# Performance work log

Hardware: AMD Instinct MI355X
Metric: run time of the kernel (lower is better)

The kernel has to match this reference:

```python
import jax, jax.numpy as jnp
import numpy as np

N_NODES = 1_000_000
N_GRAPHS = 8192
DIM = 64
FEAT = 64


def setup_inputs() -> dict:
    key = jax.random.key(0)
    ks = jax.random.split(key, 12)
    s = 0.05
    inp = {}
    inp["x"] = jax.random.normal(ks[0], (N_NODES, FEAT), jnp.float32)
    inp["batch"] = jnp.sort(jax.random.randint(ks[1], (N_NODES,), 0, N_GRAPHS, dtype=jnp.int32))
    inp["lin0_w"] = jax.random.normal(ks[2], (DIM, FEAT), jnp.float32) * s
    inp["lin0_b"] = jnp.zeros((DIM,), jnp.float32)
    inp["lin1_w"] = jax.random.normal(ks[3], (DIM, DIM), jnp.float32) * s
    inp["lin1_b"] = jnp.zeros((DIM,), jnp.float32)
    inp["gru_wih"] = jax.random.normal(ks[4], (3 * DIM, DIM), jnp.float32) * s
    inp["gru_whh"] = jax.random.normal(ks[5], (3 * DIM, DIM), jnp.float32) * s
    inp["gru_bih"] = jnp.zeros((3 * DIM,), jnp.float32)
    inp["gru_bhh"] = jnp.zeros((3 * DIM,), jnp.float32)
    inp["lstm_wih"] = jax.random.normal(ks[6], (4 * DIM, 2 * DIM), jnp.float32) * s
    inp["lstm_whh"] = jax.random.normal(ks[7], (4 * DIM, DIM), jnp.float32) * s
    inp["lstm_bih"] = jnp.zeros((4 * DIM,), jnp.float32)
    inp["lstm_bhh"] = jnp.zeros((4 * DIM,), jnp.float32)
    inp["lin2_w"] = jax.random.normal(ks[8], (DIM, 2 * DIM), jnp.float32) * s
    inp["lin2_b"] = jnp.zeros((DIM,), jnp.float32)
    inp["lin3_w"] = jax.random.normal(ks[9], (1, DIM), jnp.float32) * s
    inp["lin3_b"] = jnp.zeros((1,), jnp.float32)
    inp["n_graphs"] = N_GRAPHS
    return inp


def _gru_step(m, h, wih, whh, bih, bhh):
    # single-step PyTorch GRU semantics
    gi = m @ wih.T + bih          # [N, 3D]
    gh = h @ whh.T + bhh          # [N, 3D]
    ir, iz, in_ = jnp.split(gi, 3, axis=-1)
    hr, hz, hn = jnp.split(gh, 3, axis=-1)
    r = jax.nn.sigmoid(ir + hr)
    z = jax.nn.sigmoid(iz + hz)
    n = jnp.tanh(in_ + r * hn)
    return (1.0 - z) * n + z * h


def _segment_softmax(e, batch, n_graphs):
    m = jax.ops.segment_max(e, batch, num_segments=n_graphs)
    ex = jnp.exp(e - m[batch])
    s = jax.ops.segment_sum(ex, batch, num_segments=n_graphs)
    return ex / (s[batch] + 1e-16)


def reference(x, batch, lin0_w, lin0_b, lin1_w, lin1_b,
              gru_wih, gru_whh, gru_bih, gru_bhh,
              lstm_wih, lstm_whh, lstm_bih, lstm_bhh,
              lin2_w, lin2_b, lin3_w, lin3_b, n_graphs):
    dim = lin0_w.shape[0]
    out = jax.nn.relu(x @ lin0_w.T + lin0_b)   # [N, D]
    h = out
    for _ in range(3):
        m = jax.nn.relu(out @ lin1_w.T + lin1_b)
        h = _gru_step(m, h, gru_wih, gru_whh, gru_bih, gru_bhh)
        out = h

    # Set2Set, processing_steps = 3
    q_star = jnp.zeros((n_graphs, 2 * dim), out.dtype)
    hl = jnp.zeros((n_graphs, dim), out.dtype)
    cl = jnp.zeros((n_graphs, dim), out.dtype)
    for _ in range(3):
        gates = q_star @ lstm_wih.T + lstm_bih + hl @ lstm_whh.T + lstm_bhh  # [B, 4D]
        gi, gf, gg, go = jnp.split(gates, 4, axis=-1)
        cl = jax.nn.sigmoid(gf) * cl + jax.nn.sigmoid(gi) * jnp.tanh(gg)
        hl = jax.nn.sigmoid(go) * jnp.tanh(cl)
        q = hl                                   # [B, D]
        e = jnp.sum(out * q[batch], axis=-1)     # [N]
        a = _segment_softmax(e, batch, n_graphs) # [N]
        r = jax.ops.segment_sum(a[:, None] * out, batch, num_segments=n_graphs)  # [B, D]
        q_star = jnp.concatenate([q, r], axis=-1)

    y = jax.nn.relu(q_star @ lin2_w.T + lin2_b)
    y = y @ lin3_w.T + lin3_b
    return y.reshape(-1)
```

## Files before the change

kernel.cpp:

```cpp
#include <hip/hip_runtime.h>
#include <hip/hip_bf16.h>
#include <math.h>

#define TILES 8
#define MBLK 128

typedef __attribute__((ext_vector_type(8))) short bf8;
typedef __attribute__((ext_vector_type(4))) float f32x4;

#define MFMA(a, b, c) __builtin_amdgcn_mfma_f32_16x16x32_bf16(a, b, c, 0, 0, 0)

__device__ __forceinline__ float fast_rcp(float x) { return __builtin_amdgcn_rcpf(x); }
#if __has_builtin(__builtin_amdgcn_exp2f)
__device__ __forceinline__ float exp2b(float x) { return __builtin_amdgcn_exp2f(x); }
#else
__device__ __forceinline__ float exp2b(float x) { return exp2f(x); }
#endif
__device__ __forceinline__ float sigm2(float xp) { return fast_rcp(1.0f + exp2b(-xp)); }
__device__ __forceinline__ float tanh2s(float up) {
    return fmaf(2.0f, fast_rcp(1.0f + exp2b(-up)), -1.0f);
}
__device__ __forceinline__ float sigm(float x) { return fast_rcp(1.0f + __expf(-x)); }
__device__ __forceinline__ float tanh2(float x) { return fmaf(2.0f, fast_rcp(1.0f + __expf(-2.0f * x)), -1.0f); }

__device__ __forceinline__ unsigned short f2bf(float v) {
    union { __hip_bfloat16 b; unsigned short u; } cv;
    cv.b = __float2bfloat16(v);
    return cv.u;
}
__device__ __forceinline__ float bf2f(unsigned short u) {
    union { unsigned short u; __hip_bfloat16 b; } cv;
    cv.u = u;
    return __bfloat162float(cv.b);
}
__device__ __forceinline__ void split_tr(float v, unsigned short& hi, unsigned short& lo) {
    unsigned int uv = __builtin_bit_cast(unsigned int, v);
    hi = (unsigned short)(uv >> 16);
    float rem = v - __builtin_bit_cast(float, uv & 0xffff0000u);
    lo = f2bf(rem);
}
__device__ __forceinline__ f32x4 ntload4(const float* p) {
    return __builtin_nontemporal_load((const f32x4*)p);
}

__global__ void prep_kernel(const float* __restrict__ l0w, const float* __restrict__ l1w,
                            const float* __restrict__ gwih, const float* __restrict__ gwhh,
                            const float* __restrict__ lwih, const float* __restrict__ lwhh,
                            const float* __restrict__ l2w,
                            const int* __restrict__ batch,
                            unsigned short* __restrict__ whi, unsigned short* __restrict__ wlo,
                            float* __restrict__ liT, float* __restrict__ lhT,
                            float* __restrict__ l2T,
                            int* __restrict__ startp,
                            int n_nodes, int n_graphs)
{
    int tid = blockIdx.x * 256 + threadIdx.x;
    if (tid < 32768) {
        int e = tid & 7, lane = (tid >> 3) & 63, ks = (tid >> 9) & 1, jt = tid >> 10;
        const float* W; int jl;
        if (jt < 4)       { W = l0w;  jl = jt; }
        else if (jt < 8)  { W = l1w;  jl = jt - 4; }
        else if (jt < 20) { W = gwih; jl = jt - 8; }
        else              { W = gwhh; jl = jt - 20; }
        int j = jl * 16 + (lane & 15);
        int k = ks * 32 + (lane >> 4) * 8 + e;
        float v = W[j * 64 + k];
        if (jt >= 8) v *= (j < 128) ? 1.44269504f : 2.88539008f;
        unsigned short hi = f2bf(v);
        whi[tid] = hi;
        wlo[tid] = f2bf(v - bf2f(hi));
    }
    if (tid < 32768) liT[tid] = lwih[(tid & 255) * 128 + (tid >> 8)];
    if (tid < 16384) lhT[tid] = lwhh[(tid & 255) * 64 + (tid >> 8)];
    if (tid < 8192)  l2T[tid] = l2w[(tid & 63) * 128 + (tid >> 6)];
    if (tid <= n_graphs) {
        int lo = 0, hi = n_nodes;
        while (lo < hi) {
            int mid = (lo + hi) >> 1;
            if (batch[mid] < tid) lo = mid + 1; else hi = mid;
        }
        startp[tid] = lo;
    }
}

__launch_bounds__(256, 2)
__global__ void node_kernel(const float* __restrict__ x,
                            const unsigned short* __restrict__ whi,
                            const unsigned short* __restrict__ wlo,
                            const float* __restrict__ l0b, const float* __restrict__ l1b,
                            const float* __restrict__ gbih, const float* __restrict__ gbhh,
                            float* __restrict__ outv, int n_nodes)
{
    __shared__ unsigned short MHI[TILES * 1024], MLO[TILES * 1024];
    __shared__ unsigned short HHI[TILES * 1024], HLO[TILES * 1024];
    const int tid = threadIdx.x;
    const int w = tid >> 6, lane = tid & 63, c = lane & 15, g = lane >> 4;
    const long node0 = (long)blockIdx.x * MBLK;
    const int j = w * 16 + c;

    const float bR  = (gbih[j] + gbhh[j]) * 1.44269504f;
    const float bZ  = (gbih[64 + j] + gbhh[64 + j]) * 1.44269504f;
    const float bNI = gbih[128 + j] * 2.88539008f;
    const float bNH = gbhh[128 + j] * 2.88539008f;
    const float bL1 = l1b[j];
    const float bL0 = l0b[j];

    const int kgj = (j >> 3) & 3;
    const int koff2 = ((j >> 5) * 512) + (kgj * 128) + (j & 7);
    const int lane_swz = (lane & 48) | (c ^ g);

    const bf8* WH = (const bf8*)whi;
    const bf8* WL = (const bf8*)wlo;
#define LF(name, jt) \
    bf8 name##h0 = WH[((jt) * 2 + 0) * 64 + lane], name##h1 = WH[((jt) * 2 + 1) * 64 + lane], \
        name##l0 = WL[((jt) * 2 + 0) * 64 + lane], name##l1 = WL[((jt) * 2 + 1) * 64 + lane];
    LF(w0, w)
    LF(w1, 4 + w)
    LF(gir, 8 + w)  LF(giz, 12 + w)  LF(gin, 16 + w)
    LF(ghr, 20 + w) LF(ghz, 24 + w) LF(ghn, 28 + w)
#undef LF

    float hc[TILES][4];

#pragma unroll
    for (int t = 0; t < TILES; ++t) {
        long nd = node0 + t * 16 + c;
        if (nd >= n_nodes) nd = n_nodes - 1;
        const float* xp = x + nd * 64 + g * 8;
        float va[8], vb[8];
        {
            float4 u0 = *(const float4*)xp;
            float4 u1 = *(const float4*)(xp + 4);
            float4 u2 = *(const float4*)(xp + 32);
            float4 u3 = *(const float4*)(xp + 36);
            va[0] = u0.x; va[1] = u0.y; va[2] = u0.z; va[3] = u0.w;
            va[4] = u1.x; va[5] = u1.y; va[6] = u1.z; va[7] = u1.w;
            vb[0] = u2.x; vb[1] = u2.y; vb[2] = u2.z; vb[3] = u2.w;
            vb[4] = u3.x; vb[5] = u3.y; vb[6] = u3.z; vb[7] = u3.w;
        }
        bf8 xh0, xl0, xh1, xl1;
#pragma unroll
        for (int e = 0; e < 8; ++e) {
            unsigned short h0, l0, h1, l1;
            split_tr(va[e], h0, l0);
            split_tr(vb[e], h1, l1);
            xh0[e] = (short)h0; xl0[e] = (short)l0;
            xh1[e] = (short)h1; xl1[e] = (short)l1;
        }
        f32x4 acc = {bL0, bL0, bL0, bL0};
        acc = MFMA(xh0, w0h0, acc); acc = MFMA(xl0, w0h0, acc); acc = MFMA(xh0, w0l0, acc);
        acc = MFMA(xh1, w0h1, acc); acc = MFMA(xl1, w0h1, acc); acc = MFMA(xh1, w0l1, acc);
#pragma unroll
        for (int p = 0; p < 4; ++p) {
            float hv = fmaxf(acc[p], 0.0f);
            hc[t][p] = hv;
            int r = g * 4 + p;
            unsigned short hi, lo;
            split_tr(hv, hi, lo);
            int idx = t * 1024 + koff2 + ((r ^ kgj) << 3);
            HHI[idx] = hi;
            HLO[idx] = lo;
        }
    }
    __syncthreads();

    for (int iter = 0; iter < 3; ++iter) {
#pragma unroll
        for (int t = 0; t < TILES; ++t) {
            const bf8* hh = (const bf8*)&HHI[t * 1024];
            const bf8* hl = (const bf8*)&HLO[t * 1024];
            bf8 ah0 = hh[lane_swz], ah1 = hh[64 + lane_swz];
            bf8 al0 = hl[lane_swz], al1 = hl[64 + lane_swz];
            f32x4 acc = {bL1, bL1, bL1, bL1};
            acc = MFMA(ah0, w1h0, acc); acc = MFMA(al0, w1h0, acc); acc = MFMA(ah0, w1l0, acc);
            acc = MFMA(ah1, w1h1, acc); acc = MFMA(al1, w1h1, acc); acc = MFMA(ah1, w1l1, acc);
#pragma unroll
            for (int p = 0; p < 4; ++p) {
                float mv = fmaxf(acc[p], 0.0f);
                int r = g * 4 + p;
                unsigned short hi, lo;
                split_tr(mv, hi, lo);
                int idx = t * 1024 + koff2 + ((r ^ kgj) << 3);
                MHI[idx] = hi;
                MLO[idx] = lo;
            }
        }
        __syncthreads();

#pragma unroll
        for (int t = 0; t < TILES; ++t) {
            const bf8* mh = (const bf8*)&MHI[t * 1024];
            const bf8* ml = (const bf8*)&MLO[t * 1024];
            const bf8* hh = (const bf8*)&HHI[t * 1024];
            const bf8* hl = (const bf8*)&HLO[t * 1024];
            bf8 amh0 = mh[lane_swz], amh1 = mh[64 + lane_swz];
            bf8 aml0 = ml[lane_swz], aml1 = ml[64 + lane_swz];
            bf8 ahh0 = hh[lane_swz], ahh1 = hh[64 + lane_swz];
            bf8 ahl0 = hl[lane_swz], ahl1 = hl[64 + lane_swz];

            f32x4 aR  = {bR, bR, bR, bR};
            f32x4 aZ  = {bZ, bZ, bZ, bZ};
            f32x4 aNI = {bNI, bNI, bNI, bNI};
            f32x4 aNH = {bNH, bNH, bNH, bNH};

            aR = MFMA(amh0, girh0, aR); aR = MFMA(aml0, girh0, aR); aR = MFMA(amh0, girl0, aR);
            aR = MFMA(amh1, girh1, aR); aR = MFMA(aml1, girh1, aR); aR = MFMA(amh1, girl1, aR);
            aR = MFMA(ahh0, ghrh0, aR); aR = MFMA(ahl0, ghrh0, aR); aR = MFMA(ahh0, ghrl0, aR);
            aR = MFMA(ahh1, ghrh1, aR); aR = MFMA(ahl1, ghrh1, aR); aR = MFMA(ahh1, ghrl1, aR);

            aZ = MFMA(amh0, gizh0, aZ); aZ = MFMA(aml0, gizh0, aZ); aZ = MFMA(amh0, gizl0, aZ);
            aZ = MFMA(amh1, gizh1, aZ); aZ = MFMA(aml1, gizh1, aZ); aZ = MFMA(amh1, gizl1, aZ);
            aZ = MFMA(ahh0, ghzh0, aZ); aZ = MFMA(ahl0, ghzh0, aZ); aZ = MFMA(ahh0, ghzl0, aZ);
            aZ = MFMA(ahh1, ghzh1, aZ); aZ = MFMA(ahl1, ghzh1, aZ); aZ = MFMA(ahh1, ghzl1, aZ);

            aNI = MFMA(amh0, ginh0, aNI); aNI = MFMA(aml0, ginh0, aNI); aNI = MFMA(amh0, ginl0, aNI);
            aNI = MFMA(amh1, ginh1, aNI); aNI = MFMA(aml1, ginh1, aNI); aNI = MFMA(amh1, ginl1, aNI);

            aNH = MFMA(ahh0, ghnh0, aNH); aNH = MFMA(ahl0, ghnh0, aNH); aNH = MFMA(ahh0, ghnl0, aNH);
            aNH = MFMA(ahh1, ghnh1, aNH); aNH = MFMA(ahl1, ghnh1, aNH); aNH = MFMA(ahh1, ghnl1, aNH);

#pragma unroll
            for (int p = 0; p < 4; ++p) {
                float rg = sigm2(aR[p]);
                float zg = sigm2(aZ[p]);
                float ng = tanh2s(fmaf(rg, aNH[p], aNI[p]));
                hc[t][p] = fmaf(zg, hc[t][p] - ng, ng);
            }
        }

        if (iter < 2) {
            __syncthreads();
#pragma unroll
            for (int t = 0; t < TILES; ++t)
#pragma unroll
                for (int p = 0; p < 4; ++p) {
                    int r = g * 4 + p;
                    unsigned short hi, lo;
                    split_tr(hc[t][p], hi, lo);
                    int idx = t * 1024 + koff2 + ((r ^ kgj) << 3);
                    HHI[idx] = hi;
                    HLO[idx] = lo;
                }
            __syncthreads();
        }
    }

#pragma unroll
    for (int t = 0; t < TILES; ++t)
#pragma unroll
        for (int p = 0; p < 4; ++p) {
            long nd = node0 + t * 16 + g * 4 + p;
            if (nd < n_nodes) outv[nd * 64 + j] = hc[t][p];
        }
}

__global__ void s2s_kernel(const float* __restrict__ outv,
                           const int* __restrict__ startp,
                           const float* __restrict__ liT, const float* __restrict__ lhT,
                           const float* __restrict__ lbih, const float* __restrict__ lbhh,
                           const float* __restrict__ l2T, const float* __restrict__ l2b,
                           const float* __restrict__ l3w, const float* __restrict__ l3b,
                           float* __restrict__ yout, int n_graphs)
{
    __shared__ float uS[4][192];
    __shared__ float clS[4][64];
    __shared__ float mG[16], sG[16];
    __shared__ float rG[16][64];

    const int t = threadIdx.x;
    const int w = t >> 6, lane = t & 63;
    const int gbase = blockIdx.x * 4;
    const int grp = t >> 4, l = t & 15;

    uS[w][lane] = 0.0f; uS[w][64 + lane] = 0.0f; uS[w][128 + lane] = 0.0f;
    clS[w][lane] = 0.0f;
    __syncthreads();

    for (int step = 0; step < 3; ++step) {
        {
            const int d = lane;
            float aI = lbih[d]       + lbhh[d];
            float aF = lbih[64 + d]  + lbhh[64 + d];
            float aG = lbih[128 + d] + lbhh[128 + d];
            float aO = lbih[192 + d] + lbhh[192 + d];
            for (int k = 0; k < 128; ++k) {
                float uv = uS[w][k];
                const float* wr = liT + k * 256;
                aI = fmaf(wr[d], uv, aI);
                aF = fmaf(wr[64 + d], uv, aF);
                aG = fmaf(wr[128 + d], uv, aG);
                aO = fmaf(wr[192 + d], uv, aO);
            }
            for (int k = 0; k < 64; ++k) {
                float hv = uS[w][128 + k];
                const float* wr = lhT + k * 256;
                aI = fmaf(wr[d], hv, aI);
                aF = fmaf(wr[64 + d], hv, aF);
                aG = fmaf(wr[128 + d], hv, aG);
                aO = fmaf(wr[192 + d], hv, aO);
            }
            float c = sigm(aF) * clS[w][d] + sigm(aI) * tanh2(aG);
            clS[w][d] = c;
            float h = sigm(aO) * tanh2(c);
            uS[w][d] = h;
            uS[w][128 + d] = h;
        }
        __syncthreads();

        for (int idx = 0; idx < 4; ++idx) {
            const int g = gbase + idx;
            int s0 = 0, cnt = 0;
            if (g < n_graphs) { s0 = startp[g]; cnt = startp[g + 1] - s0; }

            const float q0 = uS[idx][l * 4 + 0], q1 = uS[idx][l * 4 + 1];
            const float q2 = uS[idx][l * 4 + 2], q3 = uS[idx][l * 4 + 3];

            float m = -INFINITY, s = 0.0f;
            float r0 = 0.0f, r1 = 0.0f, r2 = 0.0f, r3 = 0.0f;

            int n = grp;
            for (; n + 16 < cnt; n += 32) {
                f32x4 va = ntload4(outv + (size_t)(s0 + n) * 64 + l * 4);
                f32x4 vb = ntload4(outv + (size_t)(s0 + n + 16) * 64 + l * 4);
                float ea = fmaf(va.x, q0, fmaf(va.y, q1, fmaf(va.z, q2, va.w * q3)));
                float eb = fmaf(vb.x, q0, fmaf(vb.y, q1, fmaf(vb.z, q2, vb.w * q3)));
#pragma unroll
                for (int o = 1; o < 16; o <<= 1) {
                    ea += __shfl_xor(ea, o);
                    eb += __shfl_xor(eb, o);
                }
                float mn = fmaxf(m, fmaxf(ea, eb));
                float sc = __expf(m - mn);
                float wa = __expf(ea - mn);
                float wb = __expf(eb - mn);
                s = s * sc + wa + wb;
                r0 = fmaf(r0, sc, fmaf(wa, va.x, wb * vb.x));
                r1 = fmaf(r1, sc, fmaf(wa, va.y, wb * vb.y));
                r2 = fmaf(r2, sc, fmaf(wa, va.z, wb * vb.z));
                r3 = fmaf(r3, sc, fmaf(wa, va.w, wb * vb.w));
                m = mn;
            }
            if (n < cnt) {
                f32x4 va = ntload4(outv + (size_t)(s0 + n) * 64 + l * 4);
                float ea = fmaf(va.x, q0, fmaf(va.y, q1, fmaf(va.z, q2, va.w * q3)));
#pragma unroll
                for (int o = 1; o < 16; o <<= 1) ea += __shfl_xor(ea, o);
                float mn = fmaxf(m, ea);
                float sc = __expf(m - mn);
                float wa = __expf(ea - mn);
                s = s * sc + wa;
                r0 = fmaf(r0, sc, wa * va.x);
                r1 = fmaf(r1, sc, wa * va.y);
                r2 = fmaf(r2, sc, wa * va.z);
                r3 = fmaf(r3, sc, wa * va.w);
                m = mn;
            }

            if (l == 0) { mG[grp] = m; sG[grp] = s; }
            rG[grp][l * 4 + 0] = r0;
            rG[grp][l * 4 + 1] = r1;
            rG[grp][l * 4 + 2] = r2;
            rG[grp][l * 4 + 3] = r3;
            __syncthreads();

            if (t < 64) {
                float M = -INFINITY;
#pragma unroll
                for (int j2 = 0; j2 < 16; ++j2) M = fmaxf(M, mG[j2]);
                float out;
                if (M == -INFINITY) {
                    out = 0.0f;
                } else {
                    float ssum = 0.0f, racc = 0.0f;
#pragma unroll
                    for (int j2 = 0; j2 < 16; ++j2) {
                        float sc = __expf(mG[j2] - M);
                        ssum = fmaf(sG[j2], sc, ssum);
                        racc = fmaf(rG[j2][t], sc, racc);
                    }
                    out = racc / (ssum + 1e-16f);
                }
                uS[idx][64 + t] = out;
            }
            __syncthreads();
        }
    }

    {
        const int d = lane;
        float a0 = l2b[d], a1 = 0.0f, a2 = 0.0f, a3 = 0.0f;
        for (int k = 0; k < 128; k += 4) {
            a0 = fmaf(l2T[(k + 0) * 64 + d], uS[w][k + 0], a0);
            a1 = fmaf(l2T[(k + 1) * 64 + d], uS[w][k + 1], a1);
            a2 = fmaf(l2T[(k + 2) * 64 + d], uS[w][k + 2], a2);
            a3 = fmaf(l2T[(k + 3) * 64 + d], uS[w][k + 3], a3);
        }
        float y = fmaxf((a0 + a1) + (a2 + a3), 0.0f);
        float p = l3w[d] * y;
#pragma unroll
        for (int o = 32; o > 0; o >>= 1) p += __shfl_xor(p, o);
        if (d == 0 && gbase + w < n_graphs) yout[gbase + w] = p + l3b[0];
    }
}

extern "C" void kernel_launch(void* const* d_in, const int* in_sizes, int n_in,
                              void* d_out, int out_size, void* d_ws, size_t ws_size,
                              hipStream_t stream)
{
    const float* x     = (const float*)d_in[0];
    const int*   batch = (const int*)d_in[1];
    const float* l0w   = (const float*)d_in[2];
    const float* l0b   = (const float*)d_in[3];
    const float* l1w   = (const float*)d_in[4];
    const float* l1b   = (const float*)d_in[5];
    const float* gwih  = (const float*)d_in[6];
    const float* gwhh  = (const float*)d_in[7];
    const float* gbih  = (const float*)d_in[8];
    const float* gbhh  = (const float*)d_in[9];
    const float* lwih  = (const float*)d_in[10];
    const float* lwhh  = (const float*)d_in[11];
    const float* lbih  = (const float*)d_in[12];
    const float* lbhh  = (const float*)d_in[13];
    const float* l2w   = (const float*)d_in[14];
    const float* l2b   = (const float*)d_in[15];
    const float* l3w   = (const float*)d_in[16];
    const float* l3b   = (const float*)d_in[17];

    const int n_nodes  = in_sizes[1];
    const int n_graphs = out_size;

    float* wsf = (float*)d_ws;
    float* outv = wsf;
    float* liT  = wsf + (size_t)n_nodes * 64;
    float* lhT  = liT + 32768;
    float* l2T  = lhT + 16384;
    unsigned short* whi = (unsigned short*)(l2T + 8192);
    unsigned short* wlo = whi + 32768;
    int* startp = (int*)(wlo + 32768);

    prep_kernel<<<128, 256, 0, stream>>>(l0w, l1w, gwih, gwhh, lwih, lwhh, l2w, batch,
                                         whi, wlo, liT, lhT, l2T, startp,
                                         n_nodes, n_graphs);
    node_kernel<<<(n_nodes + MBLK - 1) / MBLK, 256, 0, stream>>>(
        x, whi, wlo, l0b, l1b, gbih, gbhh, outv, n_nodes);
    s2s_kernel<<<(n_graphs + 3) / 4, 256, 0, stream>>>(
        outv, startp, liT, lhT, lbih, lbhh, l2T, l2b, l3w, l3b,
        (float*)d_out, n_graphs);
}
```

Baseline: 768.5 us.

## Transpose MFMA operands so each lane owns four contiguous features for vector stores

Swaps the A/B operands of every MFMA so the accumulator holds four consecutive output features per lane instead of four nodes. This lets the hi/lo bf16 split results be written to shared memory as one short4 store instead of four scalar stores. It also lets the final output be written as one float4 global store per tile rather than scattered scalar stores. The shared-memory layout changes to an unswizzled one, which risks bank conflicts on the packed writes and on the bf8 reads.

```diff
diff --git a/kernel.cpp b/kernel.cpp
--- a/kernel.cpp
+++ b/kernel.cpp
@@ -96,18 +96,22 @@
     const int tid = threadIdx.x;
     const int w = tid >> 6, lane = tid & 63, c = lane & 15, g = lane >> 4;
     const long node0 = (long)blockIdx.x * MBLK;
-    const int j = w * 16 + c;
-
-    const float bR  = (gbih[j] + gbhh[j]) * 1.44269504f;
-    const float bZ  = (gbih[64 + j] + gbhh[64 + j]) * 1.44269504f;
-    const float bNI = gbih[128 + j] * 2.88539008f;
-    const float bNH = gbhh[128 + j] * 2.88539008f;
-    const float bL1 = l1b[j];
-    const float bL0 = l0b[j];
-
-    const int kgj = (j >> 3) & 3;
-    const int koff2 = ((j >> 5) * 512) + (kgj * 128) + (j & 7);
-    const int lane_swz = (lane & 48) | (c ^ g);
+    const int j0 = w * 16 + g * 4;
+
+    const float LOG2E = 1.44269504f;
+    float bR[4], bZ[4], bNI[4], bNH[4], bL0[4], bL1[4];
+#pragma unroll
+    for (int p = 0; p < 4; ++p) {
+        bR[p]  = (gbih[j0 + p] + gbhh[j0 + p]) * LOG2E;
+        bZ[p]  = (gbih[64 + j0 + p] + gbhh[64 + j0 + p]) * LOG2E;
+        bNI[p] = gbih[128 + j0 + p] * (2.0f * LOG2E);
+        bNH[p] = gbhh[128 + j0 + p] * (2.0f * LOG2E);
+        bL0[p] = l0b[j0 + p];
+        bL1[p] = l1b[j0 + p];
+    }
+
+    const int waddr = ((w >> 1) * 512) + (((w & 1) * 2 + (g >> 1)) * 128)
+                    + (c * 8) + ((g & 1) * 4);
 
     const bf8* WH = (const bf8*)whi;
     const bf8* WL = (const bf8*)wlo;
@@ -147,20 +151,18 @@
             xh0[e] = (short)h0; xl0[e] = (short)l0;
             xh1[e] = (short)h1; xl1[e] = (short)l1;
         }
-        f32x4 acc = {bL0, bL0, bL0, bL0};
-        acc = MFMA(xh0, w0h0, acc); acc = MFMA(xl0, w0h0, acc); acc = MFMA(xh0, w0l0, acc);
-        acc = MFMA(xh1, w0h1, acc); acc = MFMA(xl1, w0h1, acc); acc = MFMA(xh1, w0l1, acc);
+        f32x4 acc = {bL0[0], bL0[1], bL0[2], bL0[3]};
+        acc = MFMA(w0h0, xh0, acc); acc = MFMA(w0h0, xl0, acc); acc = MFMA(w0l0, xh0, acc);
+        acc = MFMA(w0h1, xh1, acc); acc = MFMA(w0h1, xl1, acc); acc = MFMA(w0l1, xh1, acc);
+        unsigned short sh[4], sl[4];
 #pragma unroll
         for (int p = 0; p < 4; ++p) {
             float hv = fmaxf(acc[p], 0.0f);
             hc[t][p] = hv;
-            int r = g * 4 + p;
-            unsigned short hi, lo;
-            split_tr(hv, hi, lo);
-            int idx = t * 1024 + koff2 + ((r ^ kgj) << 3);
-            HHI[idx] = hi;
-            HLO[idx] = lo;
-        }
+            split_tr(hv, sh[p], sl[p]);
+        }
+        *(short4*)&HHI[t * 1024 + waddr] = make_short4((short)sh[0], (short)sh[1], (short)sh[2], (short)sh[3]);
+        *(short4*)&HLO[t * 1024 + waddr] = make_short4((short)sl[0], (short)sl[1], (short)sl[2], (short)sl[3]);
     }
     __syncthreads();
 
@@ -169,21 +171,19 @@
         for (int t = 0; t < TILES; ++t) {
             const bf8* hh = (const bf8*)&HHI[t * 1024];
             const bf8* hl = (const bf8*)&HLO[t * 1024];
-            bf8 ah0 = hh[lane_swz], ah1 = hh[64 + lane_swz];
-            bf8 al0 = hl[lane_swz], al1 = hl[64 + lane_swz];
-            f32x4 acc = {bL1, bL1, bL1, bL1};
-            acc = MFMA(ah0, w1h0, acc); acc = MFMA(al0, w1h0, acc); acc = MFMA(ah0, w1l0, acc);
-            acc = MFMA(ah1, w1h1, acc); acc = MFMA(al1, w1h1, acc); acc = MFMA(ah1, w1l1, acc);
+            bf8 ah0 = hh[lane], ah1 = hh[64 + lane];
+            bf8 al0 = hl[lane], al1 = hl[64 + lane];
+            f32x4 acc = {bL1[0], bL1[1], bL1[2], bL1[3]};
+            acc = MFMA(w1h0, ah0, acc); acc = MFMA(w1h0, al0, acc); acc = MFMA(w1l0, ah0, acc);
+            acc = MFMA(w1h1, ah1, acc); acc = MFMA(w1h1, al1, acc); acc = MFMA(w1l1, ah1, acc);
+            unsigned short sh[4], sl[4];
 #pragma unroll
             for (int p = 0; p < 4; ++p) {
                 float mv = fmaxf(acc[p], 0.0f);
-                int r = g * 4 + p;
-                unsigned short hi, lo;
-                split_tr(mv, hi, lo);
-                int idx = t * 1024 + koff2 + ((r ^ kgj) << 3);
-                MHI[idx] = hi;
-                MLO[idx] = lo;
-            }
+                split_tr(mv, sh[p], sl[p]);
+            }
+            *(short4*)&MHI[t * 1024 + waddr] = make_short4((short)sh[0], (short)sh[1], (short)sh[2], (short)sh[3]);
+            *(short4*)&MLO[t * 1024 + waddr] = make_short4((short)sl[0], (short)sl[1], (short)sl[2], (short)sl[3]);
         }
         __syncthreads();
 
@@ -193,31 +193,31 @@
             const bf8* ml = (const bf8*)&MLO[t * 1024];
             const bf8* hh = (const bf8*)&HHI[t * 1024];
             const bf8* hl = (const bf8*)&HLO[t * 1024];
-            bf8 amh0 = mh[lane_swz], amh1 = mh[64 + lane_swz];
-            bf8 aml0 = ml[lane_swz], aml1 = ml[64 + lane_swz];
-            bf8 ahh0 = hh[lane_swz], ahh1 = hh[64 + lane_swz];
-            bf8 ahl0 = hl[lane_swz], ahl1 = hl[64 + lane_swz];
-
-            f32x4 aR  = {bR, bR, bR, bR};
-            f32x4 aZ  = {bZ, bZ, bZ, bZ};
-            f32x4 aNI = {bNI, bNI, bNI, bNI};
-            f32x4 aNH = {bNH, bNH, bNH, bNH};
-
-            aR = MFMA(amh0, girh0, aR); aR = MFMA(aml0, girh0, aR); aR = MFMA(amh0, girl0, aR);
-            aR = MFMA(amh1, girh1, aR); aR = MFMA(aml1, girh1, aR); aR = MFMA(amh1, girl1, aR);
-            aR = MFMA(ahh0, ghrh0, aR); aR = MFMA(ahl0, ghrh0, aR); aR = MFMA(ahh0, ghrl0, aR);
-            aR = MFMA(ahh1, ghrh1, aR); aR = MFMA(ahl1, ghrh1, aR); aR = MFMA(ahh1, ghrl1, aR);
-
-            aZ = MFMA(amh0, gizh0, aZ); aZ = MFMA(aml0, gizh0, aZ); aZ = MFMA(amh0, gizl0, aZ);
-            aZ = MFMA(amh1, gizh1, aZ); aZ = MFMA(aml1, gizh1, aZ); aZ = MFMA(amh1, gizl1, aZ);
-            aZ = MFMA(ahh0, ghzh0, aZ); aZ = MFMA(ahl0, ghzh0, aZ); aZ = MFMA(ahh0, ghzl0, aZ);
-            aZ = MFMA(ahh1, ghzh1, aZ); aZ = MFMA(ahl1, ghzh1, aZ); aZ = MFMA(ahh1, ghzl1, aZ);
-
-            aNI = MFMA(amh0, ginh0, aNI); aNI = MFMA(aml0, ginh0, aNI); aNI = MFMA(amh0, ginl0, aNI);
-            aNI = MFMA(amh1, ginh1, aNI); aNI = MFMA(aml1, ginh1, aNI); aNI = MFMA(amh1, ginl1, aNI);
-
-            aNH = MFMA(ahh0, ghnh0, aNH); aNH = MFMA(ahl0, ghnh0, aNH); aNH = MFMA(ahh0, ghnl0, aNH);
-            aNH = MFMA(ahh1, ghnh1, aNH); aNH = MFMA(ahl1, ghnh1, aNH); aNH = MFMA(ahh1, ghnl1, aNH);
+            bf8 amh0 = mh[lane], amh1 = mh[64 + lane];
+            bf8 aml0 = ml[lane], aml1 = ml[64 + lane];
+            bf8 ahh0 = hh[lane], ahh1 = hh[64 + lane];
+            bf8 ahl0 = hl[lane], ahl1 = hl[64 + lane];
+
+            f32x4 aR  = {bR[0], bR[1], bR[2], bR[3]};
+            f32x4 aZ  = {bZ[0], bZ[1], bZ[2], bZ[3]};
+            f32x4 aNI = {bNI[0], bNI[1], bNI[2], bNI[3]};
+            f32x4 aNH = {bNH[0], bNH[1], bNH[2], bNH[3]};
+
+            aR = MFMA(girh0, amh0, aR); aR = MFMA(girh0, aml0, aR); aR = MFMA(girl0, amh0, aR);
+            aR = MFMA(girh1, amh1, aR); aR = MFMA(girh1, aml1, aR); aR = MFMA(girl1, amh1, aR);
+            aR = MFMA(ghrh0, ahh0, aR); aR = MFMA(ghrh0, ahl0, aR); aR = MFMA(ghrl0, ahh0, aR);
+            aR = MFMA(ghrh1, ahh1, aR); aR = MFMA(ghrh1, ahl1, aR); aR = MFMA(ghrl1, ahh1, aR);
+
+            aZ = MFMA(gizh0, amh0, aZ); aZ = MFMA(gizh0, aml0, aZ); aZ = MFMA(gizl0, amh0, aZ);
+            aZ = MFMA(gizh1, amh1, aZ); aZ = MFMA(gizh1, aml1, aZ); aZ = MFMA(gizl1, amh1, aZ);
+            aZ = MFMA(ghzh0, ahh0, aZ); aZ = MFMA(ghzh0, ahl0, aZ); aZ = MFMA(ghzl0, ahh0, aZ);
+            aZ = MFMA(ghzh1, ahh1, aZ); aZ = MFMA(ghzh1, ahl1, aZ); aZ = MFMA(ghzl1, ahh1, aZ);
+
+            aNI = MFMA(ginh0, amh0, aNI); aNI = MFMA(ginh0, aml0, aNI); aNI = MFMA(ginl0, amh0, aNI);
+            aNI = MFMA(ginh1, amh1, aNI); aNI = MFMA(ginh1, aml1, aNI); aNI = MFMA(ginl1, amh1, aNI);
+
+            aNH = MFMA(ghnh0, ahh0, aNH); aNH = MFMA(ghnh0, ahl0, aNH); aNH = MFMA(ghnl0, ahh0, aNH);
+            aNH = MFMA(ghnh1, ahh1, aNH); aNH = MFMA(ghnh1, ahl1, aNH); aNH = MFMA(ghnl1, ahh1, aNH);
 
 #pragma unroll
             for (int p = 0; p < 4; ++p) {
@@ -231,27 +231,26 @@
         if (iter < 2) {
             __syncthreads();
 #pragma unroll
-            for (int t = 0; t < TILES; ++t)
-#pragma unroll
-                for (int p = 0; p < 4; ++p) {
-                    int r = g * 4 + p;
-                    unsigned short hi, lo;
-                    split_tr(hc[t][p], hi, lo);
-                    int idx = t * 1024 + koff2 + ((r ^ kgj) << 3);
-                    HHI[idx] = hi;
-                    HLO[idx] = lo;
-                }
+            for (int t = 0; t < TILES; ++t) {
+                unsigned short sh[4], sl[4];
+#pragma unroll
+                for (int p = 0; p < 4; ++p) split_tr(hc[t][p], sh[p], sl[p]);
+                *(short4*)&HHI[t * 1024 + waddr] = make_short4((short)sh[0], (short)sh[1], (short)sh[2], (short)sh[3]);
+                *(short4*)&HLO[t * 1024 + waddr] = make_short4((short)sl[0], (short)sl[1], (short)sl[2], (short)sl[3]);
+            }
             __syncthreads();
         }
     }
 
 #pragma unroll
-    for (int t = 0; t < TILES; ++t)
-#pragma unroll
-        for (int p = 0; p < 4; ++p) {
-            long nd = node0 + t * 16 + g * 4 + p;
-            if (nd < n_nodes) outv[nd * 64 + j] = hc[t][p];
-        }
+    for (int t = 0; t < TILES; ++t) {
+        long nd = node0 + t * 16 + c;
+        if (nd < n_nodes) {
+            float4 o;
+            o.x = hc[t][0]; o.y = hc[t][1]; o.z = hc[t][2]; o.w = hc[t][3];
+            *(float4*)(outv + nd * 64 + j0) = o;
+        }
+    }
 }
 
 __global__ void s2s_kernel(const float* __restrict__ outv,
```

Result: faster. 747.2 us (-2.8%).
